# Performance work log

Hardware: AMD Instinct MI355X
Metric: run time of the kernel (lower is better)

## Reference

```python
import jax, jax.numpy as jnp
import numpy as np

DIAG_FLOOR = 0.1
DIAG_CEIL = 1.0


def setup_inputs() -> dict:
    key = jax.random.key(0)
    k1, k2, k3, k4 = jax.random.split(key, 4)
    m, in_f, out_f = 16384, 1024, 2048
    z = jax.random.normal(k1, (m, in_f), dtype=jnp.float32)
    diag_params = jax.random.normal(k2, (out_f, in_f), dtype=jnp.float32)
    mean_params = 5.0 * jax.random.normal(k3, (out_f, in_f, 1), dtype=jnp.float32)
    scale_params = jax.random.normal(k4, (out_f,), dtype=jnp.float32)
    return {"z": z, "diag_params": diag_params, "mean_params": mean_params,
            "scale_params": scale_params}


def reference(z, diag_params, mean_params, scale_params):
    # Clamp diag to (0.1, 1.0) via sigmoid; clamp scale via tanh.
    d = DIAG_FLOOR + (DIAG_CEIL - DIAG_FLOOR) * jax.nn.sigmoid(diag_params)  # (out, in)
    mean = mean_params[..., 0]  # (out, in)

    # Diagonal covariance => quadratic forms reduce to elementwise products:
    # z_cov_z[m,k]    = sum_i d[k,i] * z[m,i]^2
    # mean_cov_mean[k]= sum_i d[k,i] * mean[k,i]^2
    # z_cov_mean[m,k] = sum_i z[m,i] * d[k,i] * mean[k,i]
    z_cov_z = jnp.einsum('mi,ki->mk', z * z, d)          # (m, out)
    mean_cov_mean = jnp.sum(d * mean * mean, axis=1)      # (out,)
    z_cov_mean = jnp.einsum('mi,ki->mk', z, d * mean)     # (m, out)

    scaling = jnp.tanh(scale_params)                      # (out,)
    return scaling * jnp.exp(-z_cov_z - mean_cov_mean + 2.0 * z_cov_mean)
```

## Files before the change

kernel.cpp:

```cpp
#include <hip/hip_runtime.h>
#include <hip/hip_bf16.h>
#include <cstdint>
#include <cstddef>

#define M_DIM 16384
#define IN_F  1024
#define OUT_F 2048
#define K_CAT 2048
#define NT    (K_CAT / 32)

typedef float f32x4 __attribute__((ext_vector_type(4)));
typedef short short8 __attribute__((ext_vector_type(8)));

__device__ __forceinline__ void gld_lds16(const void* gptr, void* lptr) {
    __builtin_amdgcn_global_load_lds(
        (const __attribute__((address_space(1))) uint32_t*)gptr,
        (__attribute__((address_space(3))) uint32_t*)lptr,
        16 , 0 , 0 );
}

__global__ __launch_bounds__(256) void prep_z_kernel(const float* __restrict__ z,
                                                     __hip_bfloat16* __restrict__ A) {
    const int idx = blockIdx.x * 256 + threadIdx.x;
    const int m  = idx >> 7;
    const int c8 = (idx & 127) * 8;
    const float4 v0 = ((const float4*)z)[idx * 2];
    const float4 v1 = ((const float4*)z)[idx * 2 + 1];
    const float x[8] = {v0.x, v0.y, v0.z, v0.w, v1.x, v1.y, v1.z, v1.w};
    __hip_bfloat16 q[8], r[8];
#pragma unroll
    for (int j = 0; j < 8; ++j) {
        q[j] = __float2bfloat16(x[j] * x[j]);
        r[j] = __float2bfloat16(x[j]);
    }
    __hip_bfloat16* rowp = A + (size_t)m * K_CAT;
    *(uint4*)&rowp[c8]        = *(uint4*)q;
    *(uint4*)&rowp[IN_F + c8] = *(uint4*)r;
}

__global__ __launch_bounds__(256) void prep_b_kernel(const float* __restrict__ diag,
                                                     const float* __restrict__ mean,
                                                     const float* __restrict__ scale,
                                                     __hip_bfloat16* __restrict__ B,
                                                     float* __restrict__ mcm,
                                                     float* __restrict__ ts) {
    const int k = blockIdx.x;
    const int t = threadIdx.x;
    const float4 dp = ((const float4*)(diag + (size_t)k * IN_F))[t];
    const float4 mp = ((const float4*)(mean + (size_t)k * IN_F))[t];
    const float dx[4] = {dp.x, dp.y, dp.z, dp.w};
    const float mx[4] = {mp.x, mp.y, mp.z, mp.w};
    __hip_bfloat16 nb[4], pb[4];
    float acc = 0.f;
#pragma unroll
    for (int j = 0; j < 4; ++j) {
        const float d = 0.1f + 0.9f / (1.f + __expf(-dx[j]));
        nb[j] = __float2bfloat16(-d);
        pb[j] = __float2bfloat16(2.f * d * mx[j]);
        acc += d * mx[j] * mx[j];
    }
    __hip_bfloat16* rowp = B + (size_t)k * K_CAT;
    *(uint2*)&rowp[t * 4]        = *(uint2*)nb;
    *(uint2*)&rowp[IN_F + t * 4] = *(uint2*)pb;
#pragma unroll
    for (int off = 32; off > 0; off >>= 1) acc += __shfl_down(acc, off);
    __shared__ float red[4];
    if ((t & 63) == 0) red[t >> 6] = acc;
    __syncthreads();
    if (t == 0) {
        mcm[k] = red[0] + red[1] + red[2] + red[3];
        ts[k]  = tanhf(scale[k]);
    }
}

__global__ __launch_bounds__(512, 2) void gemm_exp_kernel(
    const __hip_bfloat16* __restrict__ A,
    const __hip_bfloat16* __restrict__ B,
    const float* __restrict__ mcm,
    const float* __restrict__ ts,
    float* __restrict__ out) {
    __shared__ __align__(16) __hip_bfloat16 smem[4][2][8192];

    const int t = threadIdx.x;
    const int wg = ((blockIdx.x & 7) << 6) | (blockIdx.x >> 3);
    const int tn = wg & 7;
    const int tm = wg >> 3;

    const int c0 = t, c1 = t + 512;
    const int r0 = c0 >> 2, u0 = c0 & 3;
    const int r1 = c1 >> 2, u1 = c1 & 3;
    const int s0 = u0 ^ ((r0 >> 1) & 3);
    const int s1 = u1 ^ ((r1 >> 1) & 3);
    const __hip_bfloat16* gA0 = A + (size_t)(tm * 256 + r0) * K_CAT + s0 * 8;
    const __hip_bfloat16* gA1 = A + (size_t)(tm * 256 + r1) * K_CAT + s1 * 8;
    const __hip_bfloat16* gB0 = B + (size_t)(tn * 256 + r0) * K_CAT + s0 * 8;
    const __hip_bfloat16* gB1 = B + (size_t)(tn * 256 + r1) * K_CAT + s1 * 8;

#define ISSUE_A(buf_, kt_) do { \
        gld_lds16(gA0 + (kt_) * 32, &smem[buf_][0][c0 * 8]); \
        gld_lds16(gA1 + (kt_) * 32, &smem[buf_][0][c1 * 8]); } while (0)
#define ISSUE_B(buf_, kt_) do { \
        gld_lds16(gB0 + (kt_) * 32, &smem[buf_][1][c0 * 8]); \
        gld_lds16(gB1 + (kt_) * 32, &smem[buf_][1][c1 * 8]); } while (0)

    const int wid = t >> 6, lane = t & 63;
    const int wmb = (wid >> 2) * 128;
    const int wnb = (wid & 3) * 64;
    const int l15 = lane & 15, l4 = lane >> 4;
    int offA[8], offB[4];
#pragma unroll
    for (int fm = 0; fm < 8; ++fm) {
        const int r = wmb + fm * 16 + l15;
        offA[fm] = r * 32 + (l4 ^ ((r >> 1) & 3)) * 8;
    }
#pragma unroll
    for (int fn = 0; fn < 4; ++fn) {
        const int r = wnb + fn * 16 + l15;
        offB[fn] = r * 32 + (l4 ^ ((r >> 1) & 3)) * 8;
    }

    f32x4 acc[8][4] = {};

    ISSUE_A(0, 0); ISSUE_B(0, 0);
    ISSUE_A(1, 1); ISSUE_B(1, 1);
    ISSUE_A(2, 2); ISSUE_B(2, 2);
    asm volatile("s_waitcnt vmcnt(8)" ::: "memory");
    __builtin_amdgcn_s_barrier();
    __builtin_amdgcn_sched_barrier(0);

#pragma unroll 4
    for (int kt = 0; kt < NT; ++kt) {
        const int buf  = kt & 3;
        const int pf   = (kt < NT - 3) ? kt + 3 : NT - 1;
        const int pbuf = (kt + 3) & 3;

        short8 bfr[4], af[8];
#pragma unroll
        for (int fn = 0; fn < 4; ++fn) bfr[fn] = *(const short8*)&smem[buf][1][offB[fn]];
#pragma unroll
        for (int fm = 0; fm < 8; ++fm) af[fm]  = *(const short8*)&smem[buf][0][offA[fm]];
        ISSUE_A(pbuf, pf);
        ISSUE_B(pbuf, pf);
        __builtin_amdgcn_sched_barrier(0);
        asm volatile("s_waitcnt lgkmcnt(0)" ::: "memory");
        __builtin_amdgcn_sched_barrier(0);
        __builtin_amdgcn_s_setprio(1);
#pragma unroll
        for (int fm = 0; fm < 8; ++fm)
#pragma unroll
            for (int fn = 0; fn < 4; ++fn)
                acc[fm][fn] = __builtin_amdgcn_mfma_f32_16x16x32_bf16(
                    af[fm], bfr[fn], acc[fm][fn], 0, 0, 0);
        __builtin_amdgcn_s_setprio(0);
        __builtin_amdgcn_sched_barrier(0);
        asm volatile("s_waitcnt vmcnt(8)" ::: "memory");
        __builtin_amdgcn_s_barrier();
        __builtin_amdgcn_sched_barrier(0);
    }
#undef ISSUE_A
#undef ISSUE_B

#pragma unroll
    for (int fn = 0; fn < 4; ++fn) {
        const int gn = tn * 256 + wnb + fn * 16 + l15;
        const float tsv = ts[gn];
        const float mv  = mcm[gn];
#pragma unroll
        for (int fm = 0; fm < 8; ++fm) {
            const int gm0 = tm * 256 + wmb + fm * 16 + l4 * 4;
#pragma unroll
            for (int r = 0; r < 4; ++r)
                out[(size_t)(gm0 + r) * OUT_F + gn] = tsv * __expf(acc[fm][fn][r] - mv);
        }
    }
}

extern "C" void kernel_launch(void* const* d_in, const int* in_sizes, int n_in,
                              void* d_out, int out_size, void* d_ws, size_t ws_size,
                              hipStream_t stream) {
    const float* z     = (const float*)d_in[0];
    const float* diag  = (const float*)d_in[1];
    const float* mean  = (const float*)d_in[2];
    const float* scale = (const float*)d_in[3];
    float* out = (float*)d_out;

    char* ws = (char*)d_ws;
    const size_t A_BYTES = (size_t)M_DIM * K_CAT * sizeof(__hip_bfloat16);
    const size_t B_BYTES = (size_t)OUT_F * K_CAT * sizeof(__hip_bfloat16);
    __hip_bfloat16* Abuf = (__hip_bfloat16*)ws;
    __hip_bfloat16* Bbuf = (__hip_bfloat16*)(ws + A_BYTES);
    float* mcm = (float*)(ws + A_BYTES + B_BYTES);
    float* ts  = (float*)(ws + A_BYTES + B_BYTES + 8192);

    prep_z_kernel<<<(M_DIM * IN_F / 8) / 256, 256, 0, stream>>>(z, Abuf);
    prep_b_kernel<<<OUT_F, 256, 0, stream>>>(diag, mean, scale, Bbuf, mcm, ts);
    gemm_exp_kernel<<<(M_DIM / 256) * (OUT_F / 256), 512, 0, stream>>>(
        Abuf, Bbuf, mcm, ts, out);
}
```

Baseline: 315.7 us.

## Double-buffer LDS fragments in registers to overlap LDS reads with MFMA

The GEMM main loop is restructured so that while the MFMAs for tile k run on one register fragment set, the A/B fragments for tile k+1 are already being read from LDS into a second set. The loop is manually unrolled by two, alternating between the two sets. The global-load wait is tightened from vmcnt(8) to vmcnt(4) so the next tile is resident before the barrier. The goal is to hide LDS read latency behind the matrix instructions, at the cost of extra VGPRs for the second fragment set and one more tile of global-load latency exposed at each barrier.

```diff
diff --git a/kernel.cpp b/kernel.cpp
--- a/kernel.cpp
+++ b/kernel.cpp
@@ -73,6 +73,8 @@
     }
 }
 
+struct FragSet { short8 a[8]; short8 b[4]; };
+
 __global__ __launch_bounds__(512, 2) void gemm_exp_kernel(
     const __hip_bfloat16* __restrict__ A,
     const __hip_bfloat16* __restrict__ B,
@@ -120,43 +122,49 @@
     }
 
     f32x4 acc[8][4] = {};
+    FragSet fe, fo;
 
     ISSUE_A(0, 0); ISSUE_B(0, 0);
     ISSUE_A(1, 1); ISSUE_B(1, 1);
     ISSUE_A(2, 2); ISSUE_B(2, 2);
-    asm volatile("s_waitcnt vmcnt(8)" ::: "memory");
+    asm volatile("s_waitcnt vmcnt(4)" ::: "memory");
     __builtin_amdgcn_s_barrier();
     __builtin_amdgcn_sched_barrier(0);
-
-#pragma unroll 4
-    for (int kt = 0; kt < NT; ++kt) {
-        const int buf  = kt & 3;
-        const int pf   = (kt < NT - 3) ? kt + 3 : NT - 1;
-        const int pbuf = (kt + 3) & 3;
-
-        short8 bfr[4], af[8];
-#pragma unroll
-        for (int fn = 0; fn < 4; ++fn) bfr[fn] = *(const short8*)&smem[buf][1][offB[fn]];
-#pragma unroll
-        for (int fm = 0; fm < 8; ++fm) af[fm]  = *(const short8*)&smem[buf][0][offA[fm]];
-        ISSUE_A(pbuf, pf);
-        ISSUE_B(pbuf, pf);
-        __builtin_amdgcn_sched_barrier(0);
-        asm volatile("s_waitcnt lgkmcnt(0)" ::: "memory");
-        __builtin_amdgcn_sched_barrier(0);
-        __builtin_amdgcn_s_setprio(1);
-#pragma unroll
-        for (int fm = 0; fm < 8; ++fm)
-#pragma unroll
-            for (int fn = 0; fn < 4; ++fn)
-                acc[fm][fn] = __builtin_amdgcn_mfma_f32_16x16x32_bf16(
-                    af[fm], bfr[fn], acc[fm][fn], 0, 0, 0);
-        __builtin_amdgcn_s_setprio(0);
-        __builtin_amdgcn_sched_barrier(0);
-        asm volatile("s_waitcnt vmcnt(8)" ::: "memory");
-        __builtin_amdgcn_s_barrier();
-        __builtin_amdgcn_sched_barrier(0);
-    }
+#pragma unroll
+    for (int fm = 0; fm < 8; ++fm) fe.a[fm] = *(const short8*)&smem[0][0][offA[fm]];
+#pragma unroll
+    for (int fn = 0; fn < 4; ++fn) fe.b[fn] = *(const short8*)&smem[0][1][offB[fn]];
+    asm volatile("s_waitcnt lgkmcnt(0)" ::: "memory");
+    __builtin_amdgcn_sched_barrier(0);
+
+#define SUBITER(KT_, CUR_, NXT_) do {                                          \
+    const int pf_   = ((KT_) + 3 < NT) ? (KT_) + 3 : NT - 1;                   \
+    const int pbuf_ = ((KT_) + 3) & 3;                                         \
+    ISSUE_A(pbuf_, pf_); ISSUE_B(pbuf_, pf_);                                  \
+    __builtin_amdgcn_sched_barrier(0);                                         \
+    _Pragma("unroll") for (int fm = 0; fm < 8; ++fm)                           \
+        NXT_.a[fm] = *(const short8*)&smem[((KT_) + 1) & 3][0][offA[fm]];      \
+    _Pragma("unroll") for (int fn = 0; fn < 4; ++fn)                           \
+        NXT_.b[fn] = *(const short8*)&smem[((KT_) + 1) & 3][1][offB[fn]];      \
+    __builtin_amdgcn_sched_barrier(0);                                         \
+    __builtin_amdgcn_s_setprio(1);                                             \
+    _Pragma("unroll") for (int fm = 0; fm < 8; ++fm)                           \
+        _Pragma("unroll") for (int fn = 0; fn < 4; ++fn)                       \
+            acc[fm][fn] = __builtin_amdgcn_mfma_f32_16x16x32_bf16(             \
+                CUR_.a[fm], CUR_.b[fn], acc[fm][fn], 0, 0, 0);                 \
+    __builtin_amdgcn_s_setprio(0);                                             \
+    __builtin_amdgcn_sched_barrier(0);                                         \
+    asm volatile("s_waitcnt lgkmcnt(0)" ::: "memory");        \
+    asm volatile("s_waitcnt vmcnt(4)" ::: "memory");    \
+    __builtin_amdgcn_s_barrier();                                              \
+    __builtin_amdgcn_sched_barrier(0);                                         \
+} while (0)
+
+    for (int kt = 0; kt < NT; kt += 2) {
+        SUBITER(kt,     fe, fo);
+        SUBITER(kt + 1, fo, fe);
+    }
+#undef SUBITER
 #undef ISSUE_A
 #undef ISSUE_B
 
```

Result: no change. 320.5 us (+1.5%).
